# Optimization experiments

Hardware: AMD Instinct MI355X
Metric: run time of the kernel (lower is better)

## Reference

```python
import jax, jax.numpy as jnp
import numpy as np

B = 8192

def setup_inputs() -> dict:
    key = jax.random.key(0)
    k1, k2, k3 = jax.random.split(key, 3)
    pred = jax.random.normal(k1, (B,), dtype=jnp.float32)
    frac_time = jax.random.uniform(k2, (B,), dtype=jnp.float32) * 100.0
    if_mof = (jax.random.uniform(k3, (B,)) < 0.7).astype(jnp.float32)  # 0/1 flags
    gt = jnp.stack([frac_time, if_mof], axis=1)  # [B, 2]
    return {"pred": pred, "gt": gt, "gt_fracTime": 0, "gt_ifMOF": 1}


def reference(pred, gt, gt_fracTime, gt_ifMOF):
    # pred: [B], gt: [B,2]
    target = gt[:, gt_fracTime]          # [B]
    if_mof = gt[:, gt_ifMOF]             # [B], 0/1 flags
    flag = (if_mof == 1).astype(pred.dtype)
    n = pred.shape[0]
    # valid pairs: i < j with both flags set (loss term is symmetric in (i,j))
    triu = jnp.triu(jnp.ones((n, n), dtype=bool), k=1)
    pair_mask = (flag[:, None] * flag[None, :]) * triu.astype(pred.dtype)  # [B,B]
    dp = pred[:, None] - pred[None, :]      # [B,B]
    dt = target[:, None] - target[None, :]  # [B,B]
    loss = jnp.maximum(dp * dt / 100.0, 0.0)
    n_pairs = pair_mask.sum()
    return (loss * pair_mask).sum() / n_pairs
```

## Files before the change

### kernel.cpp

```cpp
#include <hip/hip_runtime.h>

#define NELEM 8192
#define JTILE 256
#define NJT   (NELEM / JTILE)
#define IBLK  512
#define NIB   (NELEM / IBLK)
#define NBLOCKS (NIB * NJT)

__global__ __launch_bounds__(256) void pair_kernel(
    const float* __restrict__ pred,
    const float* __restrict__ gt,
    const int* __restrict__ colT,
    const int* __restrict__ colF,
    float* __restrict__ ws_sum)
{
    __shared__ float2 sj[JTILE];

    const int tid = threadIdx.x;
    const int ib  = blockIdx.x;
    const int tj  = blockIdx.y;
    const int ct  = colT[0];
    const int cf  = colF[0];

    {
        const int j = tj * JTILE + tid;
        const float2 g = ((const float2*)gt)[j];
        const float tv = (ct == 0) ? g.x : g.y;
        const float fv = (cf == 0) ? g.x : g.y;
        const float pj = pred[j];
        const bool  fl = (fv == 1.0f);
        float2 e;
        e.x = fl ? pj          : -1e30f;
        e.y = fl ? tv * 0.01f  :  1e30f;
        sj[tid] = e;
    }
    __syncthreads();

    const int i0 = ib * IBLK + tid;
    const int i1 = i0 + 256;
    const float2 g0 = ((const float2*)gt)[i0];
    const float2 g1 = ((const float2*)gt)[i1];
    const float p0 = pred[i0];
    const float p1 = pred[i1];
    const float t0 = ((ct == 0) ? g0.x : g0.y) * 0.01f;
    const float t1 = ((ct == 0) ? g1.x : g1.y) * 0.01f;
    const float f0 = (((cf == 0) ? g0.x : g0.y) == 1.0f) ? 1.0f : 0.0f;
    const float f1 = (((cf == 0) ? g1.x : g1.y) == 1.0f) ? 1.0f : 0.0f;

    float a0 = 0.0f, a1 = 0.0f;
    #pragma unroll 8
    for (int jj = 0; jj < JTILE; ++jj) {
        const float2 v = sj[jj];
        a0 += fmaxf((p0 - v.x) * (t0 - v.y), 0.0f);
        a1 += fmaxf((p1 - v.x) * (t1 - v.y), 0.0f);
    }
    float s = a0 * f0 + a1 * f1;

    for (int off = 32; off > 0; off >>= 1) s += __shfl_down(s, off, 64);
    __shared__ float wsum[4];
    if ((tid & 63) == 0) wsum[tid >> 6] = s;
    __syncthreads();
    if (tid == 0) ws_sum[tj * NIB + ib] = wsum[0] + wsum[1] + wsum[2] + wsum[3];
}

__global__ __launch_bounds__(256) void finalize(
    const float* __restrict__ ws_sum,
    const float* __restrict__ gt,
    const int* __restrict__ colF,
    float* __restrict__ out)
{
    const int tid = threadIdx.x;
    const int cf  = colF[0];

    double s = 0.0;
    for (int i = tid; i < NBLOCKS; i += 256) s += (double)ws_sum[i];

    int m = 0;
    for (int i = tid; i < NELEM; i += 256) {
        const float2 g = ((const float2*)gt)[i];
        const float fv = (cf == 0) ? g.x : g.y;
        m += (fv == 1.0f) ? 1 : 0;
    }

    for (int off = 32; off > 0; off >>= 1) {
        s += __shfl_down(s, off, 64);
        m += __shfl_down(m, off, 64);
    }
    __shared__ double sd[4];
    __shared__ int    md[4];
    if ((tid & 63) == 0) { sd[tid >> 6] = s; md[tid >> 6] = m; }
    __syncthreads();
    if (tid == 0) {
        const double S = sd[0] + sd[1] + sd[2] + sd[3];
        const double M = (double)(md[0] + md[1] + md[2] + md[3]);
        out[0] = (float)(S / (M * (M - 1.0)));
    }
}

extern "C" void kernel_launch(void* const* d_in, const int* in_sizes, int n_in,
                              void* d_out, int out_size, void* d_ws, size_t ws_size,
                              hipStream_t stream) {
    const float* pred = (const float*)d_in[0];
    const float* gt   = (const float*)d_in[1];
    const int*   colT = (const int*)d_in[2];
    const int*   colF = (const int*)d_in[3];

    float* ws_sum = (float*)d_ws;

    dim3 grid(NIB, NJT);
    pair_kernel<<<grid, 256, 0, stream>>>(pred, gt, colT, colF, ws_sum);
    finalize<<<1, 256, 0, stream>>>(ws_sum, gt, colF, (float*)d_out);
}
```

Baseline: 18.22 us.

## Use |dp||dt| identity with moment sums and register-block 16 rows per thread

Rewrites the relu pair term with the identity max(x,0) = (|x|+x)/2. The inner loop now accumulates |dp|*|dt| as a single FMA per pair, and the linear part is recovered in closed form from per-block moment sums (count, Σp, Σt, Σpt, Σ|pt|). Non-flagged j entries are zeroed, and the extra contribution they add is subtracted in finalize. Each thread now keeps 16 i rows in registers against a 32-wide j tile, which raises reuse and removes the max op. The trade-off is more float cancellation when large sums are subtracted, and higher register pressure.

```diff
diff --git a/kernel.cpp b/kernel.cpp
--- a/kernel.cpp
+++ b/kernel.cpp
@@ -1,99 +1,123 @@
 #include <hip/hip_runtime.h>
 
 #define NELEM 8192
-#define JTILE 256
+#define JTILE 32
 #define NJT   (NELEM / JTILE)
-#define IBLK  512
+#define IPT   16
+#define IBLK  (256 * IPT)
 #define NIB   (NELEM / IBLK)
-#define NBLOCKS (NIB * NJT)
+#define NBLK  (NIB * NJT)
 
 __global__ __launch_bounds__(256) void pair_kernel(
     const float* __restrict__ pred,
     const float* __restrict__ gt,
     const int* __restrict__ colT,
     const int* __restrict__ colF,
-    float* __restrict__ ws_sum)
+    float* __restrict__ ws)
 {
     __shared__ float2 sj[JTILE];
-
     const int tid = threadIdx.x;
     const int ib  = blockIdx.x;
     const int tj  = blockIdx.y;
     const int ct  = colT[0];
     const int cf  = colF[0];
 
-    {
+    if (tid < JTILE) {
         const int j = tj * JTILE + tid;
         const float2 g = ((const float2*)gt)[j];
         const float tv = (ct == 0) ? g.x : g.y;
         const float fv = (cf == 0) ? g.x : g.y;
         const float pj = pred[j];
         const bool  fl = (fv == 1.0f);
-        float2 e;
-        e.x = fl ? pj          : -1e30f;
-        e.y = fl ? tv * 0.01f  :  1e30f;
-        sj[tid] = e;
+        sj[tid] = make_float2(fl ? pj : 0.0f, fl ? tv * 0.01f : 0.0f);
     }
     __syncthreads();
 
-    const int i0 = ib * IBLK + tid;
-    const int i1 = i0 + 256;
-    const float2 g0 = ((const float2*)gt)[i0];
-    const float2 g1 = ((const float2*)gt)[i1];
-    const float p0 = pred[i0];
-    const float p1 = pred[i1];
-    const float t0 = ((ct == 0) ? g0.x : g0.y) * 0.01f;
-    const float t1 = ((ct == 0) ? g1.x : g1.y) * 0.01f;
-    const float f0 = (((cf == 0) ? g0.x : g0.y) == 1.0f) ? 1.0f : 0.0f;
-    const float f1 = (((cf == 0) ? g1.x : g1.y) == 1.0f) ? 1.0f : 0.0f;
+    float p[IPT], t[IPT], f[IPT], acc[IPT];
+    #pragma unroll
+    for (int k = 0; k < IPT; ++k) {
+        const int i = ib * IBLK + k * 256 + tid;
+        const float2 g = ((const float2*)gt)[i];
+        p[k] = pred[i];
+        t[k] = ((ct == 0) ? g.x : g.y) * 0.01f;
+        f[k] = (((cf == 0) ? g.x : g.y) == 1.0f) ? 1.0f : 0.0f;
+        acc[k] = 0.0f;
+    }
 
-    float a0 = 0.0f, a1 = 0.0f;
-    #pragma unroll 8
+    #pragma unroll 4
     for (int jj = 0; jj < JTILE; ++jj) {
         const float2 v = sj[jj];
-        a0 += fmaxf((p0 - v.x) * (t0 - v.y), 0.0f);
-        a1 += fmaxf((p1 - v.x) * (t1 - v.y), 0.0f);
+        #pragma unroll
+        for (int k = 0; k < IPT; ++k)
+            acc[k] = fmaf(fabsf(p[k] - v.x), fabsf(t[k] - v.y), acc[k]);
     }
-    float s = a0 * f0 + a1 * f1;
+
+    float s = 0.0f;
+    #pragma unroll
+    for (int k = 0; k < IPT; ++k) s = fmaf(f[k], acc[k], s);
 
     for (int off = 32; off > 0; off >>= 1) s += __shfl_down(s, off, 64);
     __shared__ float wsum[4];
     if ((tid & 63) == 0) wsum[tid >> 6] = s;
     __syncthreads();
-    if (tid == 0) ws_sum[tj * NIB + ib] = wsum[0] + wsum[1] + wsum[2] + wsum[3];
+    if (tid == 0) ws[tj * NIB + ib] = wsum[0] + wsum[1] + wsum[2] + wsum[3];
+
+    if (tj == 0) {
+        float c = 0, sp = 0, st = 0, spt = 0, sab = 0;
+        #pragma unroll
+        for (int k = 0; k < IPT; ++k) {
+            const float pt = p[k] * t[k];
+            c   += f[k];
+            sp   = fmaf(f[k], p[k], sp);
+            st   = fmaf(f[k], t[k], st);
+            spt  = fmaf(f[k], pt, spt);
+            sab  = fmaf(f[k], fabsf(pt), sab);
+        }
+        for (int off = 32; off > 0; off >>= 1) {
+            c   += __shfl_down(c,   off, 64);
+            sp  += __shfl_down(sp,  off, 64);
+            st  += __shfl_down(st,  off, 64);
+            spt += __shfl_down(spt, off, 64);
+            sab += __shfl_down(sab, off, 64);
+        }
+        __shared__ float s5[4][5];
+        const int wid = tid >> 6;
+        if ((tid & 63) == 0) {
+            s5[wid][0] = c;  s5[wid][1] = sp;  s5[wid][2] = st;
+            s5[wid][3] = spt; s5[wid][4] = sab;
+        }
+        __syncthreads();
+        if (tid == 0) {
+            float* o = ws + NBLK + ib * 5;
+            #pragma unroll
+            for (int m = 0; m < 5; ++m)
+                o[m] = s5[0][m] + s5[1][m] + s5[2][m] + s5[3][m];
+        }
+    }
 }
 
 __global__ __launch_bounds__(256) void finalize(
-    const float* __restrict__ ws_sum,
-    const float* __restrict__ gt,
-    const int* __restrict__ colF,
+    const float* __restrict__ ws,
     float* __restrict__ out)
 {
     const int tid = threadIdx.x;
-    const int cf  = colF[0];
-
     double s = 0.0;
-    for (int i = tid; i < NBLOCKS; i += 256) s += (double)ws_sum[i];
-
-    int m = 0;
-    for (int i = tid; i < NELEM; i += 256) {
-        const float2 g = ((const float2*)gt)[i];
-        const float fv = (cf == 0) ? g.x : g.y;
-        m += (fv == 1.0f) ? 1 : 0;
-    }
-
-    for (int off = 32; off > 0; off >>= 1) {
-        s += __shfl_down(s, off, 64);
-        m += __shfl_down(m, off, 64);
-    }
+    for (int i = tid; i < NBLK; i += 256) s += (double)ws[i];
+    for (int off = 32; off > 0; off >>= 1) s += __shfl_down(s, off, 64);
     __shared__ double sd[4];
-    __shared__ int    md[4];
-    if ((tid & 63) == 0) { sd[tid >> 6] = s; md[tid >> 6] = m; }
+    if ((tid & 63) == 0) sd[tid >> 6] = s;
     __syncthreads();
     if (tid == 0) {
-        const double S = sd[0] + sd[1] + sd[2] + sd[3];
-        const double M = (double)(md[0] + md[1] + md[2] + md[3]);
-        out[0] = (float)(S / (M * (M - 1.0)));
+        const double Braw = sd[0] + sd[1] + sd[2] + sd[3];
+        double M = 0, P = 0, Q = 0, T = 0, D = 0;
+        for (int ib = 0; ib < NIB; ++ib) {
+            const float* o = ws + NBLK + ib * 5;
+            M += (double)o[0]; P += (double)o[1]; Q += (double)o[2];
+            T += (double)o[3]; D += (double)o[4];
+        }
+        const double A = 2.0 * (M * T - P * Q);
+        const double B = Braw - ((double)NELEM - M) * D;
+        out[0] = (float)((A + B) / (2.0 * M * (M - 1.0)));
     }
 }
 
@@ -105,9 +129,9 @@
     const int*   colT = (const int*)d_in[2];
     const int*   colF = (const int*)d_in[3];
 
-    float* ws_sum = (float*)d_ws;
+    float* ws = (float*)d_ws;
 
     dim3 grid(NIB, NJT);
-    pair_kernel<<<grid, 256, 0, stream>>>(pred, gt, colT, colF, ws_sum);
-    finalize<<<1, 256, 0, stream>>>(ws_sum, gt, colF, (float*)d_out);
+    pair_kernel<<<grid, 256, 0, stream>>>(pred, gt, colT, colF, ws);
+    finalize<<<1, 256, 0, stream>>>(ws, (float*)d_out);
 }
```

New measurement: 16.61 us. 8.8% less time.
